# Kernel tuning notes

Measured on AMD Instinct MI355X. Metric: run time of the kernel, lower is better.

Reference implementation:

```python
import jax, jax.numpy as jnp
import numpy as np

B, T, N, NIN = 2, 10, 128, 6
K, H = 4, 128          # edge_types, n_hid
E = N * (N - 1)        # fully-connected, no self-loops


def _linear_init(key, out_f, in_f, bias=True):
    k1, k2 = jax.random.split(key)
    bound = 1.0 / np.sqrt(in_f)
    W = jax.random.uniform(k1, (out_f, in_f), jnp.float32, -bound, bound)
    if bias:
        b = jax.random.uniform(k2, (out_f,), jnp.float32, -bound, bound)
        return W, b
    return W


def setup_inputs() -> dict:
    key = jax.random.key(0)
    ks = jax.random.split(key, 20)
    # graph structure: one-hot receiver/sender matrices (NRI style)
    off_diag = np.ones((N, N), dtype=np.float32) - np.eye(N, dtype=np.float32)
    send_idx, recv_idx = np.where(off_diag)
    eye = np.eye(N, dtype=np.float32)
    rel_rec = jnp.asarray(eye[recv_idx])   # [E, N]
    rel_send = jnp.asarray(eye[send_idx])  # [E, N]

    data = jax.random.normal(ks[0], (B, T, N, NIN), jnp.float32)
    rel_type = jax.nn.softmax(jax.random.normal(ks[1], (B, E, K), jnp.float32), axis=-1)

    # per-edge-type message MLPs, stacked over edge type
    m1 = [_linear_init(ks[2 + i], H, 2 * H) for i in range(K)]
    m2 = [_linear_init(ks[6 + i], H, H) for i in range(K)]
    W_msg1 = jnp.stack([w for w, _ in m1]); b_msg1 = jnp.stack([b for _, b in m1])
    W_msg2 = jnp.stack([w for w, _ in m2]); b_msg2 = jnp.stack([b for _, b in m2])

    W_hr = _linear_init(ks[10], H, H, bias=False)
    W_hi = _linear_init(ks[11], H, H, bias=False)
    W_hh = _linear_init(ks[12], H, H, bias=False)
    W_ir, b_ir = _linear_init(ks[13], H, NIN)
    W_ii, b_ii = _linear_init(ks[14], H, NIN)
    W_in, b_in = _linear_init(ks[15], H, NIN)
    W_o1, b_o1 = _linear_init(ks[16], H, H)
    W_o2, b_o2 = _linear_init(ks[17], H, H)
    W_o3, b_o3 = _linear_init(ks[18], NIN, H)

    return dict(data=data, rel_type=rel_type, rel_rec=rel_rec, rel_send=rel_send,
                W_msg1=W_msg1, b_msg1=b_msg1, W_msg2=W_msg2, b_msg2=b_msg2,
                W_hr=W_hr, W_hi=W_hi, W_hh=W_hh,
                W_ir=W_ir, b_ir=b_ir, W_ii=W_ii, b_ii=b_ii, W_in=W_in, b_in=b_in,
                W_o1=W_o1, b_o1=b_o1, W_o2=W_o2, b_o2=b_o2, W_o3=W_o3, b_o3=b_o3)


def reference(data, rel_type, rel_rec, rel_send,
              W_msg1, b_msg1, W_msg2, b_msg2,
              W_hr, W_hi, W_hh,
              W_ir, b_ir, W_ii, b_ii, W_in, b_in,
              W_o1, b_o1, W_o2, b_o2, W_o3, b_o3):
    norm = float(K)  # skip_first=False -> all edge types, norm = edge_types
    rel_type_k = jnp.transpose(rel_type, (2, 0, 1))[..., None]  # [K, B, E, 1]

    def single_step(hidden, ins):
        # gather node hidden states to edges
        receivers = jnp.einsum('en,bnh->beh', rel_rec, hidden)
        senders = jnp.einsum('en,bnh->beh', rel_send, hidden)
        pre_msg = jnp.concatenate([receivers, senders], axis=-1)  # [B, E, 2H]
        # per-edge-type 2-layer tanh MLP, batched over edge types (dropout p=0)
        msg = jnp.tanh(jnp.einsum('bef,khf->kbeh', pre_msg, W_msg1) + b_msg1[:, None, None, :])
        msg = jnp.tanh(jnp.einsum('kbeh,kgh->kbeg', msg, W_msg2) + b_msg2[:, None, None, :])
        all_msgs = jnp.sum(msg * rel_type_k, axis=0) / norm      # [B, E, H]
        # scatter-aggregate edge messages to receiver nodes
        agg = jnp.einsum('beh,en->bnh', all_msgs, rel_rec) / NIN  # [B, N, H]
        # GRU-style update
        r = jax.nn.sigmoid(ins @ W_ir.T + b_ir + agg @ W_hr.T)
        i = jax.nn.sigmoid(ins @ W_ii.T + b_ii + agg @ W_hi.T)
        n = jnp.tanh(ins @ W_in.T + b_in + r * (agg @ W_hh.T))
        hidden_new = (1.0 - i) * n + i * hidden
        # output MLP with residual (dropout p=0)
        p = jax.nn.relu(hidden_new @ W_o1.T + b_o1)
        p = jax.nn.relu(p @ W_o2.T + b_o2)
        pred = ins + p @ W_o3.T + b_o3
        return hidden_new, pred

    hidden0 = jnp.zeros((B, N, H), data.dtype)
    # pred_steps=1 (default) -> every step consumes the ground-truth frame
    ins_seq = jnp.transpose(data[:, :-1], (1, 0, 2, 3))  # [T-1, B, N, NIN]
    _, preds = jax.lax.scan(single_step, hidden0, ins_seq)
    # stack(dim=1).transpose(1,2) -> [B, N, T-1, NIN]
    return jnp.transpose(preds, (1, 2, 0, 3))
```

## Files before the change

### kernel.cpp

```cpp
#include <hip/hip_runtime.h>

#define NN 128
#define HH 128
#define BB 2
#define KT 4
#define EE 16256
#define TT 9

typedef __bf16 v8bf __attribute__((ext_vector_type(8)));
typedef float v4f __attribute__((ext_vector_type(4)));

__device__ __forceinline__ float tanh_fast(float x) {
  return 1.0f - __fdividef(2.0f, __expf(2.0f * x) + 1.0f);
}
__device__ __forceinline__ float sigmoid_fast(float x) {
  return __fdividef(1.0f, 1.0f + __expf(-x));
}
__device__ __forceinline__ unsigned short f2bf(float f) {
  unsigned int u = __float_as_uint(f);
  u += 0x7FFFu + ((u >> 16) & 1u);
  return (unsigned short)(u >> 16);
}

__global__ void prep_kernel(const float* __restrict__ W_msg1,
                            const float* __restrict__ W_msg2,
                            const float* __restrict__ rel_type,
                            unsigned short* __restrict__ W1hi,
                            unsigned short* __restrict__ W1lo,
                            unsigned short* __restrict__ W2bf,
                            float* __restrict__ relp) {
  int idx = blockIdx.x * 256 + threadIdx.x;
  {
    int h = idx & 127, g = (idx >> 7) & 127, ku = idx >> 14;
    int k = ku >> 1, u = ku & 1;
    float w = W_msg1[(k * 128 + g) * 256 + u * 128 + h];
    unsigned short hi = f2bf(w);
    float whi = __uint_as_float(((unsigned int)hi) << 16);
    W1hi[idx] = hi;
    W1lo[idx] = f2bf(w - whi);
  }
  if (idx < 65536) W2bf[idx] = f2bf(W_msg2[idx]);
  {
    int r = idx & 127, k = (idx >> 7) & 3, n = (idx >> 9) & 127, b = idx >> 16;
    float v = 0.f;
    if (r != n) {
      int e = r * 127 + (n < r ? n : n - 1);
      v = rel_type[(b * EE + e) * KT + k];
    }
    relp[idx] = v;
  }
}

__global__ __launch_bounds__(256)
void msg_kernel(const float* __restrict__ b_msg1,
                const float* __restrict__ b_msg2,
                const unsigned short* __restrict__ W2bf,
                const float* __restrict__ relp,
                const float* __restrict__ UVin,
                float* __restrict__ agg,
                int dummy) {
  __shared__ unsigned short w2_lds[16384];
  __shared__ float ub_lds[128];
  __shared__ float b2_lds[128];
  __shared__ float rel_lds[128];
  __shared__ float colsum[4][128];

  const int tid = threadIdx.x;
  const int lane = tid & 63;
  const int wave = tid >> 6;
  const int bid = blockIdx.x;
  const int k = bid & 3;
  const int n = (bid >> 2) & 127;
  const int b = bid >> 9;

  {
    const uint4* w2g = (const uint4*)(W2bf + k * 16384);
#pragma unroll
    for (int i = 0; i < 8; ++i) {
      int cid = tid + i * 256;
      int g = cid >> 4, cc = cid & 15;
      uint4 v = w2g[cid];
      int off = (g << 8) + (cc << 4);
      off ^= (g & 7) << 4;
      *(uint4*)((char*)w2_lds + off) = v;
    }
    if (tid < 128) {
      ub_lds[tid] = UVin[(((k * 2 + 0) * BB + b) * NN + n) * HH + tid] + b_msg1[k * 128 + tid];
      b2_lds[tid] = b_msg2[k * 128 + tid];
      rel_lds[tid] = relp[(b * NN + n) * (KT * NN) + k * 128 + tid];
    }
  }
  __syncthreads();

  v8bf af[2][4];
#pragma unroll
  for (int rt = 0; rt < 2; ++rt) {
    int row = wave * 32 + rt * 16 + (lane & 15);
    const float* vbase = UVin + (((k * 2 + 1) * BB + b) * NN + row) * HH;
#pragma unroll
    for (int ks = 0; ks < 4; ++ks) {
      int c0 = ks * 32 + ((lane >> 4) << 3);
      float4 v0 = *(const float4*)(vbase + c0);
      float4 v1 = *(const float4*)(vbase + c0 + 4);
      const float* up = ub_lds + c0;
      af[rt][ks][0] = (__bf16)tanh_fast(up[0] + v0.x);
      af[rt][ks][1] = (__bf16)tanh_fast(up[1] + v0.y);
      af[rt][ks][2] = (__bf16)tanh_fast(up[2] + v0.z);
      af[rt][ks][3] = (__bf16)tanh_fast(up[3] + v0.w);
      af[rt][ks][4] = (__bf16)tanh_fast(up[4] + v1.x);
      af[rt][ks][5] = (__bf16)tanh_fast(up[5] + v1.y);
      af[rt][ks][6] = (__bf16)tanh_fast(up[6] + v1.z);
      af[rt][ks][7] = (__bf16)tanh_fast(up[7] + v1.w);
    }
  }

  v4f acck[2][8];
#pragma unroll
  for (int rt = 0; rt < 2; ++rt)
#pragma unroll
    for (int c = 0; c < 8; ++c) acck[rt][c] = (v4f){0.f, 0.f, 0.f, 0.f};
#pragma unroll
  for (int ks = 0; ks < 4; ++ks) {
#pragma unroll
    for (int c = 0; c < 8; ++c) {
      int g = c * 16 + (lane & 15);
      int boff = (g << 8) + (ks << 6) + ((lane >> 4) << 4);
      boff ^= (g & 7) << 4;
      v8bf bfrag = *(const v8bf*)((const char*)w2_lds + boff);
      acck[0][c] = __builtin_amdgcn_mfma_f32_16x16x32_bf16(af[0][ks], bfrag, acck[0][c], 0, 0, 0);
      acck[1][c] = __builtin_amdgcn_mfma_f32_16x16x32_bf16(af[1][ks], bfrag, acck[1][c], 0, 0, 0);
    }
  }

#pragma unroll
  for (int c = 0; c < 8; ++c) {
    float bb = b2_lds[c * 16 + (lane & 15)];
    float s = 0.f;
#pragma unroll
    for (int rt = 0; rt < 2; ++rt) {
#pragma unroll
      for (int rg = 0; rg < 4; ++rg) {
        int row = wave * 32 + rt * 16 + ((lane >> 4) << 2) + rg;
        s += tanh_fast(acck[rt][c][rg] + bb) * rel_lds[row];
      }
    }
    s += __shfl_xor(s, 16);
    s += __shfl_xor(s, 32);
    if ((lane >> 4) == 0) colsum[wave][c * 16 + lane] = s;
  }
  __syncthreads();
  if (tid < 128) {
    float s = colsum[0][tid] + colsum[1][tid] + colsum[2][tid] + colsum[3][tid];
    atomicAdd(agg + (b * NN + n) * HH + tid, s * (1.0f / 24.0f));
  }
}

__global__ __launch_bounds__(512)
void tail_kernel(const float* __restrict__ data,
                 const float* __restrict__ W_hr,
                 const float* __restrict__ W_hi_,
                 const float* __restrict__ W_hh,
                 const float* __restrict__ W_ir, const float* __restrict__ b_ir,
                 const float* __restrict__ W_ii, const float* __restrict__ b_ii,
                 const float* __restrict__ W_in, const float* __restrict__ b_in,
                 const float* __restrict__ W_o1, const float* __restrict__ b_o1,
                 const float* __restrict__ W_o2, const float* __restrict__ b_o2,
                 const float* __restrict__ W_o3, const float* __restrict__ b_o3,
                 const unsigned short* __restrict__ W1hi,
                 const unsigned short* __restrict__ W1lo,
                 const float* __restrict__ aggIn,
                 float* __restrict__ hidden,
                 float* __restrict__ UVout,
                 float* __restrict__ outp,
                 int t) {
  __shared__ float agg_lds[128];
  __shared__ float hid_lds[128];
  __shared__ float hn_lds[128];
  __shared__ float ins_lds[6];
  __shared__ float g_r[128], g_i[128], g_hh[128], g_in[128];
  __shared__ float p1_lds[128], p2_lds[128];

  const int tid = threadIdx.x;
  const int lane = tid & 63;
  const int wave = tid >> 6;
  const int b = blockIdx.x >> 7;
  const int n = blockIdx.x & 127;

  if (tid < 128) {
    agg_lds[tid] = aggIn[(b * NN + n) * HH + tid];
    hid_lds[tid] = hidden[(b * NN + n) * HH + tid];
  }
  if (tid >= 128 && tid < 134) ins_lds[tid - 128] = data[((b * 10 + t) * NN + n) * 6 + (tid - 128)];
  __syncthreads();

  {
    int h = tid >> 2, q = tid & 3;
    const float4* whr = (const float4*)(W_hr + h * 128 + q * 32);
    const float4* whi = (const float4*)(W_hi_ + h * 128 + q * 32);
    const float4* whh = (const float4*)(W_hh + h * 128 + q * 32);
    const float4* ag4 = (const float4*)(agg_lds + q * 32);
    float phr = 0.f, phi = 0.f, phh = 0.f;
#pragma unroll
    for (int j = 0; j < 8; ++j) {
      float4 a = ag4[j];
      float4 wr = whr[j], wi = whi[j], wh = whh[j];
      phr += wr.x * a.x + wr.y * a.y + wr.z * a.z + wr.w * a.w;
      phi += wi.x * a.x + wi.y * a.y + wi.z * a.z + wi.w * a.w;
      phh += wh.x * a.x + wh.y * a.y + wh.z * a.z + wh.w * a.w;
    }
    phr += __shfl_xor(phr, 1); phr += __shfl_xor(phr, 2);
    phi += __shfl_xor(phi, 1); phi += __shfl_xor(phi, 2);
    phh += __shfl_xor(phh, 1); phh += __shfl_xor(phh, 2);
    if (q == 0) {
      float dr = b_ir[h], di = b_ii[h], dn = b_in[h];
#pragma unroll
      for (int j = 0; j < 6; ++j) {
        float iv = ins_lds[j];
        dr += W_ir[h * 6 + j] * iv;
        di += W_ii[h * 6 + j] * iv;
        dn += W_in[h * 6 + j] * iv;
      }
      g_r[h] = dr + phr; g_i[h] = di + phi; g_hh[h] = phh; g_in[h] = dn;
    }
  }
  __syncthreads();
  if (tid < 128) {
    float r = sigmoid_fast(g_r[tid]);
    float ii = sigmoid_fast(g_i[tid]);
    float ng = tanh_fast(g_in[tid] + r * g_hh[tid]);
    float hn = (1.0f - ii) * ng + ii * hid_lds[tid];
    hn_lds[tid] = hn;
    hidden[(b * NN + n) * HH + tid] = hn;
  }
  __syncthreads();

  {
    int h = tid >> 2, q = tid & 3;
    const float4* w4 = (const float4*)(W_o1 + h * 128 + q * 32);
    const float4* a4 = (const float4*)(hn_lds + q * 32);
    float p = 0.f;
#pragma unroll
    for (int j = 0; j < 8; ++j) {
      float4 w = w4[j]; float4 a = a4[j];
      p += w.x * a.x + w.y * a.y + w.z * a.z + w.w * a.w;
    }
    p += __shfl_xor(p, 1); p += __shfl_xor(p, 2);
    if (q == 0) p1_lds[h] = fmaxf(p + b_o1[h], 0.f);
  }
  __syncthreads();
  {
    int h = tid >> 2, q = tid & 3;
    const float4* w4 = (const float4*)(W_o2 + h * 128 + q * 32);
    const float4* a4 = (const float4*)(p1_lds + q * 32);
    float p = 0.f;
#pragma unroll
    for (int j = 0; j < 8; ++j) {
      float4 w = w4[j]; float4 a = a4[j];
      p += w.x * a.x + w.y * a.y + w.z * a.z + w.w * a.w;
    }
    p += __shfl_xor(p, 1); p += __shfl_xor(p, 2);
    if (q == 0) p2_lds[h] = fmaxf(p + b_o2[h], 0.f);
  }
  __syncthreads();
  if (tid < 48) {
    int i = tid >> 3, oc = tid & 7;
    const float4* w4 = (const float4*)(W_o3 + i * 128 + oc * 16);
    const float4* a4 = (const float4*)(p2_lds + oc * 16);
    float p = 0.f;
#pragma unroll
    for (int j = 0; j < 4; ++j) {
      float4 w = w4[j]; float4 a = a4[j];
      p += w.x * a.x + w.y * a.y + w.z * a.z + w.w * a.w;
    }
    p += __shfl_xor(p, 1); p += __shfl_xor(p, 2); p += __shfl_xor(p, 4);
    if (oc == 0) outp[((b * NN + n) * TT + t) * 6 + i] = ins_lds[i] + p + b_o3[i];
  }

  {
    v8bf hf_hi[4], hf_lo[4];
#pragma unroll
    for (int q = 0; q < 4; ++q) {
      int c0 = q * 32 + ((lane >> 4) << 3);
      bool live = (lane & 15) == 0;
#pragma unroll
      for (int j = 0; j < 8; ++j) {
        float a = live ? hn_lds[c0 + j] : 0.f;
        __bf16 ah = (__bf16)a;
        hf_hi[q][j] = ah;
        hf_lo[q][j] = (__bf16)(a - (float)ah);
      }
    }
#pragma unroll
    for (int c = 0; c < 8; ++c) {
      int gg = (wave * 8 + c) * 16 + (lane & 15);
      v4f acc = (v4f){0.f, 0.f, 0.f, 0.f};
#pragma unroll
      for (int q = 0; q < 4; ++q) {
        int hoff = q * 32 + ((lane >> 4) << 3);
        v8bf bhi = *(const v8bf*)(W1hi + (size_t)gg * 128 + hoff);
        v8bf blo = *(const v8bf*)(W1lo + (size_t)gg * 128 + hoff);
        acc = __builtin_amdgcn_mfma_f32_16x16x32_bf16(hf_hi[q], bhi, acc, 0, 0, 0);
        acc = __builtin_amdgcn_mfma_f32_16x16x32_bf16(hf_lo[q], bhi, acc, 0, 0, 0);
        acc = __builtin_amdgcn_mfma_f32_16x16x32_bf16(hf_hi[q], blo, acc, 0, 0, 0);
      }
      if ((lane >> 4) == 0) {
        int kh = gg >> 7, g = gg & 127;
        UVout[((kh * BB + b) * NN + n) * HH + g] = acc[0];
      }
    }
  }
}

extern "C" void kernel_launch(void* const* d_in, const int* in_sizes, int n_in,
                              void* d_out, int out_size, void* d_ws, size_t ws_size,
                              hipStream_t stream) {
  const float* data     = (const float*)d_in[0];
  const float* rel_type = (const float*)d_in[1];
  const float* W_msg1 = (const float*)d_in[4];
  const float* b_msg1 = (const float*)d_in[5];
  const float* W_msg2 = (const float*)d_in[6];
  const float* b_msg2 = (const float*)d_in[7];
  const float* W_hr = (const float*)d_in[8];
  const float* W_hi = (const float*)d_in[9];
  const float* W_hh = (const float*)d_in[10];
  const float* W_ir = (const float*)d_in[11];
  const float* b_ir = (const float*)d_in[12];
  const float* W_ii = (const float*)d_in[13];
  const float* b_ii = (const float*)d_in[14];
  const float* W_in = (const float*)d_in[15];
  const float* b_in = (const float*)d_in[16];
  const float* W_o1 = (const float*)d_in[17];
  const float* b_o1 = (const float*)d_in[18];
  const float* W_o2 = (const float*)d_in[19];
  const float* b_o2 = (const float*)d_in[20];
  const float* W_o3 = (const float*)d_in[21];
  const float* b_o3 = (const float*)d_in[22];
  float* outp = (float*)d_out;

  char* ws = (char*)d_ws;
  float* hidden        = (float*)(ws);
  float* UVa           = (float*)(ws + 131072);
  float* UVb           = (float*)(ws + 1179648);
  unsigned short* W1hi = (unsigned short*)(ws + 2228224);
  unsigned short* W1lo = (unsigned short*)(ws + 2490368);
  unsigned short* W2bf = (unsigned short*)(ws + 2752512);
  float* relp          = (float*)(ws + 2883584);
  float* aggbuf        = (float*)(ws + 3407872);

  hipMemsetAsync(hidden, 0, 131072, stream);
  hipMemsetAsync(UVa, 0, 1048576, stream);
  hipMemsetAsync(aggbuf, 0, TT * 131072, stream);
  prep_kernel<<<512, 256, 0, stream>>>(W_msg1, W_msg2, rel_type, W1hi, W1lo, W2bf, relp);

  for (int t = 0; t < TT; ++t) {
    float* uvin = (t & 1) ? UVb : UVa;
    float* uvout = (t & 1) ? UVa : UVb;
    float* agg_t = aggbuf + t * (BB * NN * HH);
    msg_kernel<<<BB * NN * KT, 256, 0, stream>>>(b_msg1, b_msg2, W2bf, relp, uvin, agg_t, 0);
    tail_kernel<<<BB * NN, 512, 0, stream>>>(
        data, W_hr, W_hi, W_hh,
        W_ir, b_ir, W_ii, b_ii, W_in, b_in,
        W_o1, b_o1, W_o2, b_o2, W_o3, b_o3,
        W1hi, W1lo, agg_t, hidden, uvout, outp, t);
  }
}
```

Before: 610.2 us.

## Fuse message and GRU tail kernels with last-block-done counter

Merges the per-step message kernel and the GRU/output tail kernel into one launch. Each of the four edge-type blocks for a node atomically bumps a per-node counter, and the last one to arrive runs the GRU update, the output MLP and the next-step UV projection, using 256 threads instead of 512. This halves the number of kernel launches per step and removes the inter-kernel barrier, so tail work can overlap with other message blocks. There is no explicit memory fence between the agg atomics and the counter increment, which leaves a small memory-ordering risk. Each tail block also does twice the per-thread work.

```diff
diff --git a/kernel.cpp b/kernel.cpp
--- a/kernel.cpp
+++ b/kernel.cpp
@@ -52,18 +52,39 @@
 }
 
 __global__ __launch_bounds__(256)
-void msg_kernel(const float* __restrict__ b_msg1,
-                const float* __restrict__ b_msg2,
-                const unsigned short* __restrict__ W2bf,
-                const float* __restrict__ relp,
-                const float* __restrict__ UVin,
-                float* __restrict__ agg,
-                int dummy) {
+void step_kernel(const float* __restrict__ data,
+                 const float* __restrict__ b_msg1,
+                 const float* __restrict__ b_msg2,
+                 const float* __restrict__ W_hr,
+                 const float* __restrict__ W_hi_,
+                 const float* __restrict__ W_hh,
+                 const float* __restrict__ W_ir, const float* __restrict__ b_ir,
+                 const float* __restrict__ W_ii, const float* __restrict__ b_ii,
+                 const float* __restrict__ W_in, const float* __restrict__ b_in,
+                 const float* __restrict__ W_o1, const float* __restrict__ b_o1,
+                 const float* __restrict__ W_o2, const float* __restrict__ b_o2,
+                 const float* __restrict__ W_o3, const float* __restrict__ b_o3,
+                 const unsigned short* __restrict__ W1hi,
+                 const unsigned short* __restrict__ W1lo,
+                 const unsigned short* __restrict__ W2bf,
+                 const float* __restrict__ relp,
+                 float* __restrict__ hidden,
+                 const float* __restrict__ UVin,
+                 float* __restrict__ UVout,
+                 float* __restrict__ agg,
+                 unsigned* __restrict__ cnt,
+                 float* __restrict__ outp,
+                 int t) {
   __shared__ unsigned short w2_lds[16384];
   __shared__ float ub_lds[128];
   __shared__ float b2_lds[128];
   __shared__ float rel_lds[128];
   __shared__ float colsum[4][128];
+  __shared__ float hn_lds[128];
+  __shared__ float gg4[4][128];
+  __shared__ float p_lds[2][128];
+  __shared__ float ins_lds[8];
+  __shared__ unsigned is_last;
 
   const int tid = threadIdx.x;
   const int lane = tid & 63;
@@ -72,6 +93,7 @@
   const int k = bid & 3;
   const int n = (bid >> 2) & 127;
   const int b = bid >> 9;
+  const int bn = b * NN + n;
 
   {
     const uint4* w2g = (const uint4*)(W2bf + k * 16384);
@@ -87,7 +109,7 @@
     if (tid < 128) {
       ub_lds[tid] = UVin[(((k * 2 + 0) * BB + b) * NN + n) * HH + tid] + b_msg1[k * 128 + tid];
       b2_lds[tid] = b_msg2[k * 128 + tid];
-      rel_lds[tid] = relp[(b * NN + n) * (KT * NN) + k * 128 + tid];
+      rel_lds[tid] = relp[bn * (KT * NN) + k * 128 + tid];
     }
   }
   __syncthreads();
@@ -151,66 +173,44 @@
   __syncthreads();
   if (tid < 128) {
     float s = colsum[0][tid] + colsum[1][tid] + colsum[2][tid] + colsum[3][tid];
-    atomicAdd(agg + (b * NN + n) * HH + tid, s * (1.0f / 24.0f));
-  }
-}
-
-__global__ __launch_bounds__(512)
-void tail_kernel(const float* __restrict__ data,
-                 const float* __restrict__ W_hr,
-                 const float* __restrict__ W_hi_,
-                 const float* __restrict__ W_hh,
-                 const float* __restrict__ W_ir, const float* __restrict__ b_ir,
-                 const float* __restrict__ W_ii, const float* __restrict__ b_ii,
-                 const float* __restrict__ W_in, const float* __restrict__ b_in,
-                 const float* __restrict__ W_o1, const float* __restrict__ b_o1,
-                 const float* __restrict__ W_o2, const float* __restrict__ b_o2,
-                 const float* __restrict__ W_o3, const float* __restrict__ b_o3,
-                 const unsigned short* __restrict__ W1hi,
-                 const unsigned short* __restrict__ W1lo,
-                 const float* __restrict__ aggIn,
-                 float* __restrict__ hidden,
-                 float* __restrict__ UVout,
-                 float* __restrict__ outp,
-                 int t) {
-  __shared__ float agg_lds[128];
-  __shared__ float hid_lds[128];
-  __shared__ float hn_lds[128];
-  __shared__ float ins_lds[6];
-  __shared__ float g_r[128], g_i[128], g_hh[128], g_in[128];
-  __shared__ float p1_lds[128], p2_lds[128];
-
-  const int tid = threadIdx.x;
-  const int lane = tid & 63;
-  const int wave = tid >> 6;
-  const int b = blockIdx.x >> 7;
-  const int n = blockIdx.x & 127;
-
+    atomicAdd(agg + bn * HH + tid, s * (1.0f / 24.0f));
+  }
+  __syncthreads();
+
+  if (tid == 0) {
+    unsigned old = atomicAdd(cnt + bn, 1u);
+    is_last = (old == KT - 1) ? 1u : 0u;
+  }
+  __syncthreads();
+  if (!is_last) return;
+
+  float* agg_l = colsum[0];
+  float* hid_l = colsum[1];
   if (tid < 128) {
-    agg_lds[tid] = aggIn[(b * NN + n) * HH + tid];
-    hid_lds[tid] = hidden[(b * NN + n) * HH + tid];
+    agg_l[tid] = agg[bn * HH + tid];
+    hid_l[tid] = hidden[bn * HH + tid];
   }
   if (tid >= 128 && tid < 134) ins_lds[tid - 128] = data[((b * 10 + t) * NN + n) * 6 + (tid - 128)];
   __syncthreads();
 
   {
-    int h = tid >> 2, q = tid & 3;
-    const float4* whr = (const float4*)(W_hr + h * 128 + q * 32);
-    const float4* whi = (const float4*)(W_hi_ + h * 128 + q * 32);
-    const float4* whh = (const float4*)(W_hh + h * 128 + q * 32);
-    const float4* ag4 = (const float4*)(agg_lds + q * 32);
+    int h = tid >> 1, q = tid & 1;
+    const float4* whr = (const float4*)(W_hr + h * 128 + q * 64);
+    const float4* whi = (const float4*)(W_hi_ + h * 128 + q * 64);
+    const float4* whh = (const float4*)(W_hh + h * 128 + q * 64);
+    const float4* ag4 = (const float4*)(agg_l + q * 64);
     float phr = 0.f, phi = 0.f, phh = 0.f;
 #pragma unroll
-    for (int j = 0; j < 8; ++j) {
+    for (int j = 0; j < 16; ++j) {
       float4 a = ag4[j];
       float4 wr = whr[j], wi = whi[j], wh = whh[j];
       phr += wr.x * a.x + wr.y * a.y + wr.z * a.z + wr.w * a.w;
       phi += wi.x * a.x + wi.y * a.y + wi.z * a.z + wi.w * a.w;
       phh += wh.x * a.x + wh.y * a.y + wh.z * a.z + wh.w * a.w;
     }
-    phr += __shfl_xor(phr, 1); phr += __shfl_xor(phr, 2);
-    phi += __shfl_xor(phi, 1); phi += __shfl_xor(phi, 2);
-    phh += __shfl_xor(phh, 1); phh += __shfl_xor(phh, 2);
+    phr += __shfl_xor(phr, 1);
+    phi += __shfl_xor(phi, 1);
+    phh += __shfl_xor(phh, 1);
     if (q == 0) {
       float dr = b_ir[h], di = b_ii[h], dn = b_in[h];
 #pragma unroll
@@ -220,52 +220,52 @@
         di += W_ii[h * 6 + j] * iv;
         dn += W_in[h * 6 + j] * iv;
       }
-      g_r[h] = dr + phr; g_i[h] = di + phi; g_hh[h] = phh; g_in[h] = dn;
+      gg4[0][h] = dr + phr; gg4[1][h] = di + phi; gg4[2][h] = phh; gg4[3][h] = dn;
     }
   }
   __syncthreads();
   if (tid < 128) {
-    float r = sigmoid_fast(g_r[tid]);
-    float ii = sigmoid_fast(g_i[tid]);
-    float ng = tanh_fast(g_in[tid] + r * g_hh[tid]);
-    float hn = (1.0f - ii) * ng + ii * hid_lds[tid];
+    float r = sigmoid_fast(gg4[0][tid]);
+    float ii = sigmoid_fast(gg4[1][tid]);
+    float ng = tanh_fast(gg4[3][tid] + r * gg4[2][tid]);
+    float hn = (1.0f - ii) * ng + ii * hid_l[tid];
     hn_lds[tid] = hn;
-    hidden[(b * NN + n) * HH + tid] = hn;
-  }
-  __syncthreads();
-
-  {
-    int h = tid >> 2, q = tid & 3;
-    const float4* w4 = (const float4*)(W_o1 + h * 128 + q * 32);
-    const float4* a4 = (const float4*)(hn_lds + q * 32);
+    hidden[bn * HH + tid] = hn;
+  }
+  __syncthreads();
+
+  {
+    int h = tid >> 1, q = tid & 1;
+    const float4* w4 = (const float4*)(W_o1 + h * 128 + q * 64);
+    const float4* a4 = (const float4*)(hn_lds + q * 64);
     float p = 0.f;
 #pragma unroll
-    for (int j = 0; j < 8; ++j) {
+    for (int j = 0; j < 16; ++j) {
       float4 w = w4[j]; float4 a = a4[j];
       p += w.x * a.x + w.y * a.y + w.z * a.z + w.w * a.w;
     }
-    p += __shfl_xor(p, 1); p += __shfl_xor(p, 2);
-    if (q == 0) p1_lds[h] = fmaxf(p + b_o1[h], 0.f);
-  }
-  __syncthreads();
-  {
-    int h = tid >> 2, q = tid & 3;
-    const float4* w4 = (const float4*)(W_o2 + h * 128 + q * 32);
-    const float4* a4 = (const float4*)(p1_lds + q * 32);
+    p += __shfl_xor(p, 1);
+    if (q == 0) p_lds[0][h] = fmaxf(p + b_o1[h], 0.f);
+  }
+  __syncthreads();
+  {
+    int h = tid >> 1, q = tid & 1;
+    const float4* w4 = (const float4*)(W_o2 + h * 128 + q * 64);
+    const float4* a4 = (const float4*)(p_lds[0] + q * 64);
     float p = 0.f;
 #pragma unroll
-    for (int j = 0; j < 8; ++j) {
+    for (int j = 0; j < 16; ++j) {
       float4 w = w4[j]; float4 a = a4[j];
       p += w.x * a.x + w.y * a.y + w.z * a.z + w.w * a.w;
     }
-    p += __shfl_xor(p, 1); p += __shfl_xor(p, 2);
-    if (q == 0) p2_lds[h] = fmaxf(p + b_o2[h], 0.f);
+    p += __shfl_xor(p, 1);
+    if (q == 0) p_lds[1][h] = fmaxf(p + b_o2[h], 0.f);
   }
   __syncthreads();
   if (tid < 48) {
     int i = tid >> 3, oc = tid & 7;
     const float4* w4 = (const float4*)(W_o3 + i * 128 + oc * 16);
-    const float4* a4 = (const float4*)(p2_lds + oc * 16);
+    const float4* a4 = (const float4*)(p_lds[1] + oc * 16);
     float p = 0.f;
 #pragma unroll
     for (int j = 0; j < 4; ++j) {
@@ -273,7 +273,7 @@
       p += w.x * a.x + w.y * a.y + w.z * a.z + w.w * a.w;
     }
     p += __shfl_xor(p, 1); p += __shfl_xor(p, 2); p += __shfl_xor(p, 4);
-    if (oc == 0) outp[((b * NN + n) * TT + t) * 6 + i] = ins_lds[i] + p + b_o3[i];
+    if (oc == 0) outp[(bn * TT + t) * 6 + i] = ins_lds[i] + p + b_o3[i];
   }
 
   {
@@ -291,8 +291,8 @@
       }
     }
 #pragma unroll
-    for (int c = 0; c < 8; ++c) {
-      int gg = (wave * 8 + c) * 16 + (lane & 15);
+    for (int c = 0; c < 16; ++c) {
+      int gg = (wave * 16 + c) * 16 + (lane & 15);
       v4f acc = (v4f){0.f, 0.f, 0.f, 0.f};
 #pragma unroll
       for (int q = 0; q < 4; ++q) {
@@ -346,21 +346,22 @@
   unsigned short* W2bf = (unsigned short*)(ws + 2752512);
   float* relp          = (float*)(ws + 2883584);
   float* aggbuf        = (float*)(ws + 3407872);
+  unsigned* cntbuf     = (unsigned*)(ws + 4587520);
 
   hipMemsetAsync(hidden, 0, 131072, stream);
   hipMemsetAsync(UVa, 0, 1048576, stream);
   hipMemsetAsync(aggbuf, 0, TT * 131072, stream);
+  hipMemsetAsync(cntbuf, 0, TT * 1024, stream);
   prep_kernel<<<512, 256, 0, stream>>>(W_msg1, W_msg2, rel_type, W1hi, W1lo, W2bf, relp);
 
   for (int t = 0; t < TT; ++t) {
     float* uvin = (t & 1) ? UVb : UVa;
     float* uvout = (t & 1) ? UVa : UVb;
-    float* agg_t = aggbuf + t * (BB * NN * HH);
-    msg_kernel<<<BB * NN * KT, 256, 0, stream>>>(b_msg1, b_msg2, W2bf, relp, uvin, agg_t, 0);
-    tail_kernel<<<BB * NN, 512, 0, stream>>>(
-        data, W_hr, W_hi, W_hh,
+    step_kernel<<<BB * NN * KT, 256, 0, stream>>>(
+        data, b_msg1, b_msg2, W_hr, W_hi, W_hh,
         W_ir, b_ir, W_ii, b_ii, W_in, b_in,
         W_o1, b_o1, W_o2, b_o2, W_o3, b_o3,
-        W1hi, W1lo, agg_t, hidden, uvout, outp, t);
-  }
-}
+        W1hi, W1lo, W2bf, relp, hidden, uvin, uvout,
+        aggbuf + t * (BB * NN * HH), cntbuf + t * (BB * NN), outp, t);
+  }
+}
```

New measurement: 1.135 ms. 85.9% more time.
